# Performance work log

Hardware: AMD Instinct MI355X
Metric: run time of the kernel (lower is better)

The kernel has to match this reference:

```python
import jax, jax.numpy as jnp
import numpy as np

INPUT_DIM = 512
HIDDEN_DIM = 1024
N, L = 128, 512


def setup_inputs() -> dict:
    key = jax.random.key(0)
    ks = jax.random.split(key, 17)
    d = {"X": jax.random.normal(ks[0], (N, L, INPUT_DIM), dtype=jnp.float32)}
    bd = 1.0 / np.sqrt(HIDDEN_DIM)
    for gi, g in enumerate(["i", "f", "g", "o"]):
        d[f"lam_{g}"] = jax.random.normal(ks[1 + 4 * gi], (HIDDEN_DIM,), dtype=jnp.float32) * 0.02
        d[f"binv_{g}"] = jnp.zeros((HIDDEN_DIM,), dtype=jnp.float32)
        d[f"W_{g}"] = jax.random.uniform(ks[2 + 4 * gi], (HIDDEN_DIM, HIDDEN_DIM), dtype=jnp.float32, minval=-bd, maxval=bd)
        d[f"b_{g}"] = jax.random.uniform(ks[3 + 4 * gi], (HIDDEN_DIM,), dtype=jnp.float32, minval=-bd, maxval=bd)
    return d


def reference(X, lam_i, binv_i, W_i, b_i, lam_f, binv_f, W_f, b_f,
              lam_g, binv_g, W_g, b_g, lam_o, binv_o, W_o, b_o):
    # G-invariant layer (DeepSets invariant): y = lambda * sum_over_features(x) + b
    s = jnp.sum(X, axis=-1, keepdims=True)           # (N, L, 1)
    pre_i = s * lam_i + binv_i                       # (N, L, H)
    pre_f = s * lam_f + binv_f
    pre_g = s * lam_g + binv_g
    pre_o = s * lam_o + binv_o
    # time-major for scan: (L, N, H)
    xs = (jnp.swapaxes(pre_i, 0, 1), jnp.swapaxes(pre_f, 0, 1),
          jnp.swapaxes(pre_g, 0, 1), jnp.swapaxes(pre_o, 0, 1))
    n = X.shape[0]
    h0 = jnp.zeros((n, HIDDEN_DIM), dtype=X.dtype)
    c0 = jnp.zeros((n, HIDDEN_DIM), dtype=X.dtype)

    def step(carry, inp):
        h, c = carry
        pi, pf, pg, po = inp
        i = jax.nn.sigmoid(pi + h @ W_i.T + b_i)
        f = jax.nn.sigmoid(pf + h @ W_f.T + b_f)
        g = jax.nn.sigmoid(pg + h @ W_g.T + b_g)   # note: sigmoid, as in source
        o = jax.nn.sigmoid(po + h @ W_o.T + b_o)
        c_new = f * c + i * g                      # at t=0, c=0 => i*g, matching source
        h_new = o * jax.nn.sigmoid(c_new)          # c activation is sigmoid in source
        return (h_new, c_new), h_new

    _, out = jax.lax.scan(step, (h0, c0), xs)       # out: (L, N, H)
    return jnp.swapaxes(out, 0, 1)                  # (N, L, H)
```

## Files before the change

### kernel.cpp

```cpp
#include <hip/hip_runtime.h>
#include <cstdint>
#include <cstddef>

#define NN 128
#define LL 512
#define DD 512
#define HH 1024
#define NJ 4096
#define ASTR 1024
#define BSTR 2048
#define NCH 8

#define AHI 0
#define BHI 4096
#define BLO 12288
#define BUFS 20480

typedef __attribute__((ext_vector_type(8))) short short8;
typedef __attribute__((ext_vector_type(4))) float f32x4;

__device__ __forceinline__ unsigned short f2bf(float x) {
  union { float f; unsigned u; } v; v.f = x;
  unsigned r = v.u + 0x7FFFu + ((v.u >> 16) & 1u);
  return (unsigned short)(r >> 16);
}
__device__ __forceinline__ float bf2f(unsigned short b) {
  union { unsigned u; float f; } v; v.u = ((unsigned)b) << 16;
  return v.f;
}
__device__ __forceinline__ float sigf(float x) { return 1.0f / (1.0f + __expf(-x)); }

__device__ __forceinline__ void glds16(const void* g, const void* l) {
  __builtin_amdgcn_global_load_lds(
      (const __attribute__((address_space(1))) unsigned int*)g,
      (__attribute__((address_space(3))) unsigned int*)l, 16, 0, 0);
}

__global__ __launch_bounds__(256)
void sum_rows_kernel(const float* __restrict__ X, float* __restrict__ sT) {
  int row  = blockIdx.x * 4 + (threadIdx.x >> 6);
  int lane = threadIdx.x & 63;
  const float* x = X + (size_t)row * DD + lane * 8;
  float4 a = *(const float4*)x;
  float4 b = *(const float4*)(x + 4);
  float v = (a.x + a.y) + (a.z + a.w) + (b.x + b.y) + (b.z + b.w);
#pragma unroll
  for (int off = 32; off > 0; off >>= 1) v += __shfl_down(v, off, 64);
  if (lane == 0) {
    int n = row >> 9, l = row & 511;
    sT[l * NN + n] = v;
  }
}

__global__ __launch_bounds__(256)
void wsplit_kernel(const float* __restrict__ Wi, const float* __restrict__ Wf,
                   const float* __restrict__ Wg, const float* __restrict__ Wo,
                   unsigned short* __restrict__ B) {
  int idx = blockIdx.x * 256 + threadIdx.x;
  int j = idx >> 7;
  int k = (idx & 127) << 3;
  int hc = j >> 2, g = j & 3;
  const float* W = (g == 0) ? Wi : (g == 1) ? Wf : (g == 2) ? Wg : Wo;
  const float4 x0 = *(const float4*)(W + (size_t)hc * HH + k);
  const float4 x1 = *(const float4*)(W + (size_t)hc * HH + k + 4);
  float xv[8] = {x0.x, x0.y, x0.z, x0.w, x1.x, x1.y, x1.z, x1.w};
  unsigned short* dhi = B + (size_t)j * BSTR + k;
  unsigned short* dlo = dhi + 1024;
#pragma unroll
  for (int e = 0; e < 8; ++e) {
    unsigned short hi = f2bf(xv[e]);
    dhi[e] = hi;
    dlo[e] = f2bf(xv[e] - bf2f(hi));
  }
}

__global__ __launch_bounds__(256)
void pack_kernel(const float* li, const float* lf, const float* lg, const float* lo_,
                 const float* bvi, const float* bvf, const float* bvg, const float* bvo,
                 const float* bi, const float* bf_, const float* bg, const float* bo,
                 float* __restrict__ lamP, float* __restrict__ biasP) {
  int j = blockIdx.x * 256 + threadIdx.x;
  int hc = j >> 2, g = j & 3;
  const float* lam = (g == 0) ? li : (g == 1) ? lf : (g == 2) ? lg : lo_;
  const float* bv  = (g == 0) ? bvi : (g == 1) ? bvf : (g == 2) ? bvg : bvo;
  const float* bb  = (g == 0) ? bi : (g == 1) ? bf_ : (g == 2) ? bg : bo;
  lamP[j] = lam[hc];
  biasP[j] = bv[hc] + bb[hc];
}

__global__ __launch_bounds__(256)
void t0_kernel(const float* __restrict__ sT, const float* __restrict__ lamP,
               const float* __restrict__ biasP, float* __restrict__ out,
               float* __restrict__ cbuf, unsigned short* __restrict__ A0) {
  int id = blockIdx.x * 256 + threadIdx.x;
  int n = id >> 10, hc = id & 1023;
  float sv = sT[n];
  float4 lam = *(const float4*)(lamP + 4 * hc);
  float4 bia = *(const float4*)(biasP + 4 * hc);
  float vi = sigf(sv * lam.x + bia.x);
  float vg = sigf(sv * lam.z + bia.z);
  float vo = sigf(sv * lam.w + bia.w);
  float cn = vi * vg;
  float hn = vo * sigf(cn);
  cbuf[n * HH + hc] = cn;
  out[(size_t)n * (LL * HH) + hc] = hn;
  A0[(size_t)n * ASTR + hc] = f2bf(hn);
}

__global__ __launch_bounds__(256, 1)
void step_kernel(const unsigned short* __restrict__ Aprev,
                 const unsigned short* __restrict__ Bbuf,
                 const float* __restrict__ sT, const float* __restrict__ lamP,
                 const float* __restrict__ biasP, float* __restrict__ out,
                 float* __restrict__ cbuf, unsigned short* __restrict__ Acur, int t)
{
  __shared__ alignas(16) short lds[2][BUFS];

  const int tid = threadIdx.x;
  const int ln  = tid & 63;
  const int w   = tid >> 6;

  const int bid = blockIdx.x;
  const int wl  = (bid & 7) * 32 + (bid >> 3);
  const int Nt  = wl >> 2;
  const int Mt  = wl & 3;
  const int n0  = Mt * 32;
  const int j0  = Nt * 64;

  const char* srcb[10];
  int ldsoff[10];
  {
    const int ps = ln & 15;
    const int rr = ln >> 4;
#pragma unroll
    for (int i = 0; i < 10; ++i) {
      int p = w * 10 + i;
      const char* s; int off;
      if (p < 8)       { int r = p * 4 + rr;        int sp = (ps & 8) | ((ps ^ r) & 7);
                         s = (const char*)(Aprev + (size_t)(n0 + r) * ASTR + sp * 8);
                         off = AHI + p * 512; }
      else if (p < 24) { int r = (p - 8) * 4 + rr;  int sp = (ps & 8) | ((ps ^ r) & 7);
                         s = (const char*)(Bbuf + (size_t)(j0 + r) * BSTR + sp * 8);
                         off = BHI + (p - 8) * 512; }
      else             { int r = (p - 24) * 4 + rr; int sp = (ps & 8) | ((ps ^ r) & 7);
                         s = (const char*)(Bbuf + (size_t)(j0 + r) * BSTR + 1024 + sp * 8);
                         off = BLO + (p - 24) * 512; }
      srcb[i] = s; ldsoff[i] = off;
    }
  }

  int aoff[2][4], boff[4];
#pragma unroll
  for (int mf = 0; mf < 2; ++mf)
#pragma unroll
    for (int sl = 0; sl < 4; ++sl) {
      int rA = mf * 16 + (ln & 15);
      int s  = sl * 4 + (ln >> 4);
      aoff[mf][sl] = rA * 128 + (((s & 8) | ((s ^ rA) & 7)) << 3);
    }
  {
    int rB = w * 16 + (ln & 15);
#pragma unroll
    for (int sl = 0; sl < 4; ++sl) {
      int s = sl * 4 + (ln >> 4);
      boff[sl] = rB * 128 + (((s & 8) | ((s ^ rB) & 7)) << 3);
    }
  }

  const int jj = j0 + w * 16 + (ln & 15);
  const float lamv = lamP[jj];
  const float biav = biasP[jj];
  const int rbase = (ln >> 4) * 4;
  const int hc = jj >> 2;
  float cold[2][4], svp[2][4];
#pragma unroll
  for (int mf = 0; mf < 2; ++mf)
#pragma unroll
    for (int r = 0; r < 4; ++r) {
      const int m = n0 + mf * 16 + rbase + r;
      cold[mf][r] = cbuf[m * HH + hc];
      svp[mf][r]  = sT[t * NN + m];
    }

  f32x4 acc0 = {0.f,0.f,0.f,0.f};
  f32x4 acc1 = {0.f,0.f,0.f,0.f};

  auto stage = [&](int c, int b) {
    const int co = c * 256;
#pragma unroll
    for (int i = 0; i < 10; ++i) glds16(srcb[i] + co, &lds[b][ldsoff[i]]);
  };

  stage(0, 0);
#pragma unroll
  for (int c = 0; c < NCH; ++c) {
    const int b = c & 1;
    __builtin_amdgcn_s_barrier();
    if (c < NCH - 1) {
      stage(c + 1, b ^ 1);
      asm volatile("s_waitcnt vmcnt(10)" ::: "memory");
    } else {
      asm volatile("s_waitcnt vmcnt(0)" ::: "memory");
    }
    __builtin_amdgcn_s_barrier();
#pragma unroll
    for (int sl = 0; sl < 4; ++sl) {
      short8 a0 = *(const short8*)&lds[b][AHI + aoff[0][sl]];
      short8 a1 = *(const short8*)&lds[b][AHI + aoff[1][sl]];
      short8 bh = *(const short8*)&lds[b][BHI + boff[sl]];
      short8 bl = *(const short8*)&lds[b][BLO + boff[sl]];
      acc0 = __builtin_amdgcn_mfma_f32_16x16x32_bf16(a0, bh, acc0, 0, 0, 0);
      acc0 = __builtin_amdgcn_mfma_f32_16x16x32_bf16(a0, bl, acc0, 0, 0, 0);
      acc1 = __builtin_amdgcn_mfma_f32_16x16x32_bf16(a1, bh, acc1, 0, 0, 0);
      acc1 = __builtin_amdgcn_mfma_f32_16x16x32_bf16(a1, bl, acc1, 0, 0, 0);
    }
  }

#pragma unroll
  for (int mf = 0; mf < 2; ++mf) {
    const int m0 = n0 + mf * 16 + rbase;
#pragma unroll
    for (int r = 0; r < 4; ++r) {
      const int m = m0 + r;
      float a = (mf == 0) ? acc0[r] : acc1[r];
      float v = sigf(a + svp[mf][r] * lamv + biav);
      const int base = ln & ~3;
      float vi = __shfl(v, base + 0, 64);
      float vf = __shfl(v, base + 1, 64);
      float vg = __shfl(v, base + 2, 64);
      float vo = __shfl(v, base + 3, 64);
      if ((ln & 3) == 0) {
        float cn = vf * cold[mf][r] + vi * vg;
        float hn = vo * sigf(cn);
        cbuf[m * HH + hc] = cn;
        out[(size_t)m * (LL * HH) + (size_t)t * HH + hc] = hn;
        Acur[(size_t)m * ASTR + hc] = f2bf(hn);
      }
    }
  }
}

extern "C" void kernel_launch(void* const* d_in, const int* in_sizes, int n_in,
                              void* d_out, int out_size, void* d_ws, size_t ws_size,
                              hipStream_t stream) {
  const float* X    = (const float*)d_in[0];
  const float* lami = (const float*)d_in[1];
  const float* bvi  = (const float*)d_in[2];
  const float* Wi   = (const float*)d_in[3];
  const float* bi   = (const float*)d_in[4];
  const float* lamf = (const float*)d_in[5];
  const float* bvf  = (const float*)d_in[6];
  const float* Wf   = (const float*)d_in[7];
  const float* bf_  = (const float*)d_in[8];
  const float* lamg = (const float*)d_in[9];
  const float* bvg  = (const float*)d_in[10];
  const float* bg   = (const float*)d_in[12];
  const float* Wg   = (const float*)d_in[11];
  const float* lamo = (const float*)d_in[13];
  const float* bvo  = (const float*)d_in[14];
  const float* Wo   = (const float*)d_in[15];
  const float* bo   = (const float*)d_in[16];

  float* out  = (float*)d_out;

  float* cbuf  = (float*)d_ws;
  float* sT    = cbuf + (size_t)NN * HH;
  float* lamP  = sT + (size_t)NN * LL;
  float* biasP = lamP + NJ;
  unsigned short* A0 = (unsigned short*)(biasP + NJ);
  unsigned short* A1 = A0 + (size_t)NN * ASTR;
  unsigned short* Bb = A1 + (size_t)NN * ASTR;

  sum_rows_kernel<<<(NN * LL) / 4, 256, 0, stream>>>(X, sT);
  wsplit_kernel<<<(NJ * 128) / 256, 256, 0, stream>>>(Wi, Wf, Wg, Wo, Bb);
  pack_kernel<<<NJ / 256, 256, 0, stream>>>(lami, lamf, lamg, lamo,
                                            bvi, bvf, bvg, bvo,
                                            bi, bf_, bg, bo, lamP, biasP);
  t0_kernel<<<(NN * HH) / 256, 256, 0, stream>>>(sT, lamP, biasP, out, cbuf, A0);

  for (int t = 1; t < LL; ++t) {
    const unsigned short* Ap = (t & 1) ? A0 : A1;
    unsigned short* Ac = (t & 1) ? (unsigned short*)A1 : A0;
    step_kernel<<<256, 256, 0, stream>>>(Ap, Bb, sT, lamP, biasP, out, cbuf, Ac, t);
  }
}
```

Baseline: 4.381 ms.

## Switch recurrent GEMM from split-bf16 weights to single fp16 operands

```diff
diff --git a/kernel.cpp b/kernel.cpp
--- a/kernel.cpp
+++ b/kernel.cpp
@@ -8,25 +8,18 @@
 #define HH 1024
 #define NJ 4096
 #define ASTR 1024
-#define BSTR 2048
-#define NCH 8
+#define BSTR 1024
+#define NCH 4
 
 #define AHI 0
-#define BHI 4096
-#define BLO 12288
-#define BUFS 20480
-
-typedef __attribute__((ext_vector_type(8))) short short8;
+#define BHI 8192
+#define BUFS 24576
+
+typedef __attribute__((ext_vector_type(8))) _Float16 half8;
 typedef __attribute__((ext_vector_type(4))) float f32x4;
 
-__device__ __forceinline__ unsigned short f2bf(float x) {
-  union { float f; unsigned u; } v; v.f = x;
-  unsigned r = v.u + 0x7FFFu + ((v.u >> 16) & 1u);
-  return (unsigned short)(r >> 16);
-}
-__device__ __forceinline__ float bf2f(unsigned short b) {
-  union { unsigned u; float f; } v; v.u = ((unsigned)b) << 16;
-  return v.f;
+__device__ __forceinline__ unsigned short f2h(float x) {
+  union { _Float16 h; unsigned short u; } v; v.h = (_Float16)x; return v.u;
 }
 __device__ __forceinline__ float sigf(float x) { return 1.0f / (1.0f + __expf(-x)); }
 
@@ -53,9 +46,9 @@
 }
 
 __global__ __launch_bounds__(256)
-void wsplit_kernel(const float* __restrict__ Wi, const float* __restrict__ Wf,
-                   const float* __restrict__ Wg, const float* __restrict__ Wo,
-                   unsigned short* __restrict__ B) {
+void wpack_kernel(const float* __restrict__ Wi, const float* __restrict__ Wf,
+                  const float* __restrict__ Wg, const float* __restrict__ Wo,
+                  unsigned short* __restrict__ B) {
   int idx = blockIdx.x * 256 + threadIdx.x;
   int j = idx >> 7;
   int k = (idx & 127) << 3;
@@ -64,14 +57,9 @@
   const float4 x0 = *(const float4*)(W + (size_t)hc * HH + k);
   const float4 x1 = *(const float4*)(W + (size_t)hc * HH + k + 4);
   float xv[8] = {x0.x, x0.y, x0.z, x0.w, x1.x, x1.y, x1.z, x1.w};
-  unsigned short* dhi = B + (size_t)j * BSTR + k;
-  unsigned short* dlo = dhi + 1024;
-#pragma unroll
-  for (int e = 0; e < 8; ++e) {
-    unsigned short hi = f2bf(xv[e]);
-    dhi[e] = hi;
-    dlo[e] = f2bf(xv[e] - bf2f(hi));
-  }
+  unsigned short* d = B + (size_t)j * BSTR + k;
+#pragma unroll
+  for (int e = 0; e < 8; ++e) d[e] = f2h(xv[e]);
 }
 
 __global__ __launch_bounds__(256)
@@ -104,7 +92,7 @@
   float hn = vo * sigf(cn);
   cbuf[n * HH + hc] = cn;
   out[(size_t)n * (LL * HH) + hc] = hn;
-  A0[(size_t)n * ASTR + hc] = f2bf(hn);
+  A0[(size_t)n * ASTR + hc] = f2h(hn);
 }
 
 __global__ __launch_bounds__(256, 1)
@@ -127,43 +115,41 @@
   const int n0  = Mt * 32;
   const int j0  = Nt * 64;
 
-  const char* srcb[10];
-  int ldsoff[10];
+  const char* srcb[12];
+  int ldsoff[12];
   {
     const int ps = ln & 15;
     const int rr = ln >> 4;
 #pragma unroll
-    for (int i = 0; i < 10; ++i) {
-      int p = w * 10 + i;
+    for (int i = 0; i < 12; ++i) {
+      int sub = i >= 6;
+      int p = w * 6 + (i - sub * 6);
       const char* s; int off;
-      if (p < 8)       { int r = p * 4 + rr;        int sp = (ps & 8) | ((ps ^ r) & 7);
-                         s = (const char*)(Aprev + (size_t)(n0 + r) * ASTR + sp * 8);
-                         off = AHI + p * 512; }
-      else if (p < 24) { int r = (p - 8) * 4 + rr;  int sp = (ps & 8) | ((ps ^ r) & 7);
-                         s = (const char*)(Bbuf + (size_t)(j0 + r) * BSTR + sp * 8);
-                         off = BHI + (p - 8) * 512; }
-      else             { int r = (p - 24) * 4 + rr; int sp = (ps & 8) | ((ps ^ r) & 7);
-                         s = (const char*)(Bbuf + (size_t)(j0 + r) * BSTR + 1024 + sp * 8);
-                         off = BLO + (p - 24) * 512; }
+      if (p < 8)  { int r = p * 4 + rr;       int sp = (ps & 8) | ((ps ^ r) & 7);
+                    s = (const char*)(Aprev + (size_t)(n0 + r) * ASTR + sub * 128 + sp * 8);
+                    off = AHI + sub * 4096 + p * 512; }
+      else        { int pb = p - 8;  int r = pb * 4 + rr;
+                    int sp = (ps & 8) | ((ps ^ r) & 7);
+                    s = (const char*)(Bbuf + (size_t)(j0 + r) * BSTR + sub * 128 + sp * 8);
+                    off = BHI + sub * 8192 + pb * 512; }
       srcb[i] = s; ldsoff[i] = off;
     }
   }
 
-  int aoff[2][4], boff[4];
-#pragma unroll
-  for (int mf = 0; mf < 2; ++mf)
-#pragma unroll
-    for (int sl = 0; sl < 4; ++sl) {
-      int rA = mf * 16 + (ln & 15);
-      int s  = sl * 4 + (ln >> 4);
-      aoff[mf][sl] = rA * 128 + (((s & 8) | ((s ^ rA) & 7)) << 3);
-    }
+  int aoff[2][8], boff[8];
   {
-    int rB = w * 16 + (ln & 15);
-#pragma unroll
-    for (int sl = 0; sl < 4; ++sl) {
-      int s = sl * 4 + (ln >> 4);
-      boff[sl] = rB * 128 + (((s & 8) | ((s ^ rB) & 7)) << 3);
+    const int hs = ln >> 4;
+#pragma unroll
+    for (int sl = 0; sl < 8; ++sl) {
+      int sub = sl >> 2;
+      int s   = (sl & 3) * 4 + hs;
+#pragma unroll
+      for (int mf = 0; mf < 2; ++mf) {
+        int rA = mf * 16 + (ln & 15);
+        aoff[mf][sl] = AHI + sub * 4096 + rA * 128 + (((s & 8) | ((s ^ rA) & 7)) << 3);
+      }
+      int rB = w * 16 + (ln & 15);
+      boff[sl] = BHI + sub * 8192 + rB * 128 + (((s & 8) | ((s ^ rB) & 7)) << 3);
     }
   }
 
@@ -186,9 +172,9 @@
   f32x4 acc1 = {0.f,0.f,0.f,0.f};
 
   auto stage = [&](int c, int b) {
-    const int co = c * 256;
-#pragma unroll
-    for (int i = 0; i < 10; ++i) glds16(srcb[i] + co, &lds[b][ldsoff[i]]);
+    const int co = c * 512;
+#pragma unroll
+    for (int i = 0; i < 12; ++i) glds16(srcb[i] + co, &lds[b][ldsoff[i]]);
   };
 
   stage(0, 0);
@@ -198,21 +184,18 @@
     __builtin_amdgcn_s_barrier();
     if (c < NCH - 1) {
       stage(c + 1, b ^ 1);
-      asm volatile("s_waitcnt vmcnt(10)" ::: "memory");
+      asm volatile("s_waitcnt vmcnt(12)" ::: "memory");
     } else {
       asm volatile("s_waitcnt vmcnt(0)" ::: "memory");
     }
     __builtin_amdgcn_s_barrier();
 #pragma unroll
-    for (int sl = 0; sl < 4; ++sl) {
-      short8 a0 = *(const short8*)&lds[b][AHI + aoff[0][sl]];
-      short8 a1 = *(const short8*)&lds[b][AHI + aoff[1][sl]];
-      short8 bh = *(const short8*)&lds[b][BHI + boff[sl]];
-      short8 bl = *(const short8*)&lds[b][BLO + boff[sl]];
-      acc0 = __builtin_amdgcn_mfma_f32_16x16x32_bf16(a0, bh, acc0, 0, 0, 0);
-      acc0 = __builtin_amdgcn_mfma_f32_16x16x32_bf16(a0, bl, acc0, 0, 0, 0);
-      acc1 = __builtin_amdgcn_mfma_f32_16x16x32_bf16(a1, bh, acc1, 0, 0, 0);
-      acc1 = __builtin_amdgcn_mfma_f32_16x16x32_bf16(a1, bl, acc1, 0, 0, 0);
+    for (int sl = 0; sl < 8; ++sl) {
+      half8 a0 = *(const half8*)&lds[b][aoff[0][sl]];
+      half8 a1 = *(const half8*)&lds[b][aoff[1][sl]];
+      half8 bb = *(const half8*)&lds[b][boff[sl]];
+      acc0 = __builtin_amdgcn_mfma_f32_16x16x32_f16(a0, bb, acc0, 0, 0, 0);
+      acc1 = __builtin_amdgcn_mfma_f32_16x16x32_f16(a1, bb, acc1, 0, 0, 0);
     }
   }
 
@@ -234,7 +217,7 @@
         float hn = vo * sigf(cn);
         cbuf[m * HH + hc] = cn;
         out[(size_t)m * (LL * HH) + (size_t)t * HH + hc] = hn;
-        Acur[(size_t)m * ASTR + hc] = f2bf(hn);
+        Acur[(size_t)m * ASTR + hc] = f2h(hn);
       }
     }
   }
@@ -254,8 +237,8 @@
   const float* bf_  = (const float*)d_in[8];
   const float* lamg = (const float*)d_in[9];
   const float* bvg  = (const float*)d_in[10];
+  const float* Wg   = (const float*)d_in[11];
   const float* bg   = (const float*)d_in[12];
-  const float* Wg   = (const float*)d_in[11];
   const float* lamo = (const float*)d_in[13];
   const float* bvo  = (const float*)d_in[14];
   const float* Wo   = (const float*)d_in[15];
@@ -272,7 +255,7 @@
   unsigned short* Bb = A1 + (size_t)NN * ASTR;
 
   sum_rows_kernel<<<(NN * LL) / 4, 256, 0, stream>>>(X, sT);
-  wsplit_kernel<<<(NJ * 128) / 256, 256, 0, stream>>>(Wi, Wf, Wg, Wo, Bb);
+  wpack_kernel<<<(NJ * 128) / 256, 256, 0, stream>>>(Wi, Wf, Wg, Wo, Bb);
   pack_kernel<<<NJ / 256, 256, 0, stream>>>(lami, lamf, lamg, lamo,
                                             bvi, bvf, bvg, bvo,
                                             bi, bf_, bg, bo, lamP, biasP);
```

New measurement: 3.564 ms. 1.23x faster.
